# Kernel optimization log

Hardware: AMD Instinct MI355X
Metric: run time of the kernel (lower is better)

Reference implementation:

```python
import jax, jax.numpy as jnp
import numpy as np

B, C, T, H, W = 1, 512, 8, 48, 48
GROUPS = 32
EPS = 1e-6


def setup_inputs() -> dict:
    key = jax.random.key(0)
    ks = jax.random.split(key, 6)
    s = 0.02  # init scale for projection weights
    return {
        "x": jax.random.normal(ks[0], (B, C, T, H, W), dtype=jnp.float32),
        "gamma": jnp.ones((C,), dtype=jnp.float32),
        "beta": jnp.zeros((C,), dtype=jnp.float32),
        "wq": jax.random.normal(ks[1], (C, C), dtype=jnp.float32) * s,
        "bq": jnp.zeros((C,), dtype=jnp.float32),
        "wk": jax.random.normal(ks[2], (C, C), dtype=jnp.float32) * s,
        "bk": jnp.zeros((C,), dtype=jnp.float32),
        "wv": jax.random.normal(ks[3], (C, C), dtype=jnp.float32) * s,
        "bv": jnp.zeros((C,), dtype=jnp.float32),
        "wo": jax.random.normal(ks[4], (C, C), dtype=jnp.float32) * s,
        "bo": jnp.zeros((C,), dtype=jnp.float32),
    }


def _group_norm(x, gamma, beta):
    b, c, t, h, w = x.shape
    xg = x.reshape(b, GROUPS, c // GROUPS, t, h, w)
    mu = xg.mean(axis=(2, 3, 4, 5), keepdims=True)
    var = xg.var(axis=(2, 3, 4, 5), keepdims=True)
    xn = ((xg - mu) * jax.lax.rsqrt(var + EPS)).reshape(b, c, t, h, w)
    return xn * gamma[None, :, None, None, None] + beta[None, :, None, None, None]


def _proj(h, wgt, bias):
    # CausalConv3d with kernel_size=1 == pointwise channel linear
    return jnp.einsum('oc,bcthw->bothw', wgt, h) + bias[None, :, None, None, None]


def reference(x, gamma, beta, wq, bq, wk, bk, wv, bv, wo, bo):
    hn = _group_norm(x, gamma, beta)
    q = _proj(hn, wq, bq)
    k = _proj(hn, wk, bk)
    v = _proj(hn, wv, bv)
    b, c, t, h, w = q.shape
    n = h * w
    # per-frame spatial attention: (b, t, n, c)
    qf = q.transpose(0, 2, 3, 4, 1).reshape(b, t, n, c)
    kf = k.transpose(0, 2, 3, 4, 1).reshape(b, t, n, c)
    vf = v.transpose(0, 2, 3, 4, 1).reshape(b, t, n, c)
    scores = jnp.einsum('btqc,btkc->btqk', qf, kf) * (c ** -0.5)
    attn = jax.nn.softmax(scores, axis=-1)
    of = jnp.einsum('btqk,btkc->btqc', attn, vf)
    o = of.reshape(b, t, h, w, c).transpose(0, 4, 1, 2, 3)
    o = _proj(o, wo, bo)
    return x + o
```

## Files before the change

### kernel.cpp

```cpp
#include <hip/hip_runtime.h>
#include <hip/hip_bf16.h>
#include <cstdint>
#include <type_traits>

typedef __attribute__((ext_vector_type(8))) __bf16 bf16x8;
typedef __attribute__((ext_vector_type(4))) float f32x4;
typedef __attribute__((ext_vector_type(2))) long longx2;

struct bf2frag { bf16x8 k0, k1; };

__device__ __forceinline__ float bf2f(unsigned short u) {
  union { uint32_t i; float f; } v; v.i = (uint32_t)u << 16; return v.f;
}
__device__ __forceinline__ unsigned short f2bf(float f) {
  union { float f; uint32_t i; } v{f};
  uint32_t r = v.i + 0x7fffu + ((v.i >> 16) & 1u);
  return (unsigned short)(r >> 16);
}

__device__ __forceinline__ void gll(const void* g, void* l) {
  __builtin_amdgcn_global_load_lds(
      (const __attribute__((address_space(1))) uint32_t*)(uintptr_t)g,
      (__attribute__((address_space(3))) uint32_t*)(uint32_t)(uintptr_t)l,
      16, 0, 0);
}

__device__ __forceinline__ void bar() {
  asm volatile("" ::: "memory");
  __builtin_amdgcn_s_barrier();
  asm volatile("" ::: "memory");
}

#define VMCNT(n) asm volatile("s_waitcnt vmcnt(" #n ")" ::: "memory")

template <int N>
__device__ __forceinline__ void vmw() {
  if constexpr (N == 0) { VMCNT(0); }
  else if constexpr (N == 1) { VMCNT(1); }
  else if constexpr (N == 2) { VMCNT(2); }
  else if constexpr (N == 3) { VMCNT(3); }
  else if constexpr (N == 4) { VMCNT(4); }
  else if constexpr (N == 5) { VMCNT(5); }
  else if constexpr (N == 6) { VMCNT(6); }
  else if constexpr (N == 7) { VMCNT(7); }
  else if constexpr (N == 8) { VMCNT(8); }
  else if constexpr (N == 9) { VMCNT(9); }
  else if constexpr (N == 10) { VMCNT(10); }
  else { VMCNT(12); }
}

__device__ __forceinline__ f32x4 mma(bf16x8 a, bf16x8 b, f32x4 c) {
  return __builtin_amdgcn_mfma_f32_16x16x32_bf16(a, b, c, 0, 0, 0);
}
__device__ __forceinline__ f32x4 mma(long a, long b, f32x4 c) {
  return __builtin_amdgcn_mfma_f32_16x16x32_fp8_fp8(a, b, c, 0, 0, 0);
}
__device__ __forceinline__ f32x4 mmak(const bf2frag& a, const bf2frag& b, f32x4 c, int k2) {
  return k2 ? mma(a.k1, b.k1, c) : mma(a.k0, b.k0, c);
}
__device__ __forceinline__ f32x4 mmak(longx2 a, longx2 b, f32x4 c, int k2) {
  return mma(a[k2], b[k2], c);
}

__device__ __forceinline__ int perm64(int m) {
  return (m & ~63) | (((m >> 3) & 3) << 4) | (((m >> 5) & 1) << 3) | (m & 7);
}

__global__ __launch_bounds__(256) void stats_partial_k(const float* __restrict__ x,
                                                       float* __restrict__ part) {
  const int g = blockIdx.x >> 3, p = blockIdx.x & 7;
  const float* base = x + (long)g * 16 * 18432 + (long)p * 2304;
  float s = 0.f, ss = 0.f;
  for (int idx = threadIdx.x; idx < 16 * 576; idx += 256) {
    const int c = idx / 576, i4 = idx % 576;
    const float4 v = *(const float4*)(base + (long)c * 18432 + i4 * 4);
    s += v.x + v.y + v.z + v.w;
    ss += v.x * v.x + v.y * v.y + v.z * v.z + v.w * v.w;
  }
  __shared__ float rs[256], rss[256];
  rs[threadIdx.x] = s; rss[threadIdx.x] = ss;
  __syncthreads();
  for (int o = 128; o > 0; o >>= 1) {
    if ((int)threadIdx.x < o) { rs[threadIdx.x] += rs[threadIdx.x + o]; rss[threadIdx.x] += rss[threadIdx.x + o]; }
    __syncthreads();
  }
  if (threadIdx.x == 0) { part[blockIdx.x * 2] = rs[0]; part[blockIdx.x * 2 + 1] = rss[0]; }
}

__global__ __launch_bounds__(256) void gn_transpose_k(const float* __restrict__ x,
                                                      const float* __restrict__ part,
                                                      const float* __restrict__ gamma,
                                                      const float* __restrict__ beta,
                                                      unsigned short* __restrict__ hnT) {
  __shared__ float tile[64][65];
  __shared__ float sm[4], sr[4];
  const int c0 = blockIdx.x * 64, n0 = blockIdx.y * 64;
  const int tn = threadIdx.x & 63, tr = threadIdx.x >> 6;
  if (threadIdx.x < 4) {
    const int g = (c0 >> 4) + threadIdx.x;
    float s = 0.f, ss = 0.f;
    for (int p = 0; p < 8; ++p) { s += part[(g * 8 + p) * 2]; ss += part[(g * 8 + p) * 2 + 1]; }
    const float mean = s / 294912.0f;
    const float var = ss / 294912.0f - mean * mean;
    sm[threadIdx.x] = mean;
    sr[threadIdx.x] = rsqrtf(var + 1e-6f);
  }
  __syncthreads();
  for (int cc = tr; cc < 64; cc += 4) {
    const int c = c0 + cc;
    const float mean = sm[cc >> 4], rstd = sr[cc >> 4];
    const float v = x[(long)c * 18432 + n0 + tn];
    tile[cc][tn] = (v - mean) * rstd * gamma[c] + beta[c];
  }
  __syncthreads();
  for (int nn = tr; nn < 64; nn += 4) {
    hnT[(long)(n0 + nn) * 512 + c0 + tn] = f2bf(tile[tn][nn]);
  }
}

__global__ __launch_bounds__(256) void pack4_bf16_k(const float* __restrict__ w0,
                                                    const float* __restrict__ w1,
                                                    const float* __restrict__ w2,
                                                    const float* __restrict__ w3,
                                                    unsigned short* __restrict__ o0,
                                                    unsigned short* __restrict__ o1,
                                                    unsigned short* __restrict__ o2,
                                                    unsigned short* __restrict__ o3,
                                                    const float* __restrict__ bq,
                                                    const float* __restrict__ bk,
                                                    float* __restrict__ bqk) {
  const int y = blockIdx.y;
  if (y == 4) {
    if (blockIdx.x == 0) {
      const int i = threadIdx.x * 4;
#pragma unroll
      for (int j = 0; j < 4; ++j) {
        const int t = i + j;
        bqk[t] = (t < 512) ? bq[t] : bk[t - 512];
      }
    }
    return;
  }
  const float* w = (y == 0) ? w0 : (y == 1) ? w1 : (y == 2) ? w2 : w3;
  unsigned short* o = (y == 0) ? o0 : (y == 1) ? o1 : (y == 2) ? o2 : o3;
  const int i = (blockIdx.x * 256 + threadIdx.x) * 4;
  const float4 v = *(const float4*)(w + i);
  ushort4 u; u.x = f2bf(v.x); u.y = f2bf(v.y); u.z = f2bf(v.z); u.w = f2bf(v.w);
  *(ushort4*)(o + i) = u;
}

template <int BM, int BIAS_MODE, int OUT_MODE, int STATS, int SCALEN, int MODE, int FP8, int P2,
          int WL = 0, int KU = 1>
__global__ __launch_bounds__((BM == 256 || WL == 2) ? 512 : 256, (WL == 1 && FP8) ? (KU == 2 ? 2 : 4) : 2)
void gemm256(const void* __restrict__ A, long lda, long sAz,
             const void* __restrict__ B, long ldb, long sBz,
             void* __restrict__ Cp, long ldc, long sCz,
             const float* __restrict__ bias,
             const float* __restrict__ resid,
             float* __restrict__ rowsums,
             const float* __restrict__ linv,
             float alpha, int K, int gx, int gy) {
  static_assert(KU == 1 || FP8, "KU=2 only on fp8 path");
  constexpr int EB = FP8 ? 1 : 2;
  constexpr int THREADS = (BM == 256 || WL == 2) ? 512 : 256;
  constexpr int BN = WL ? 128 : 256;
  constexpr int BK = 64 * KU;
  constexpr int HBA = (BM / 2) * BK * EB;
  constexpr int HBB = (BN / 2) * BK * EB;
  constexpr int HBA0 = HBA / KU, HBB0 = HBB / KU;
  constexpr int GA = HBA / (THREADS * 16);
  constexpr int GB = HBB / (THREADS * 16);
  constexpr int GA0 = GA / KU, GB0 = GB / KU;
  constexpr int V0 = GB + 2 * GA, V3 = 2 * GB + GA, VP = GB + GA;
  constexpr int NSLOT = WL ? 8 : ((BM == 256) ? 8 : 4);
  constexpr int NSLOTP = NSLOT + 1;
  constexpr int MR = WL ? 4 : 8;
  constexpr int NR = (WL == 2) ? 2 : 4;
  constexpr int FQ = WL ? 2 : 4;
  constexpr int PRIO = !P2;
  __shared__ alignas(16) unsigned char As[2][2][HBA];
  __shared__ alignas(16) unsigned char Bs[2][2][HBB];
  __shared__ float linvs[SCALEN == 2 ? BN : 1];
  using ABt2 = typename std::conditional<FP8, longx2, bf2frag>::type;

  const int tid = threadIdx.x;
  const int lane = tid & 63, wid = tid >> 6;
  const int wm = (WL == 2) ? (wid >> 2) : (WL ? (wid >> 1) : ((BM == 256) ? (wid & 1) : 0));
  const int wn = (WL == 2) ? (wid & 3) : (WL ? (wid & 1) : ((BM == 256) ? (wid >> 1) : wid));
  int bx, by, bz;
  const void* Asel = A;
  const void* Bsel = B;
  void* Csel = Cp;
  const float* biasSel = bias;
  long ldcSel = ldc;
  bool bias_m = (BIAS_MODE == 1);
  {
    const int g8 = blockIdx.x & 7, n = blockIdx.x >> 3;
    if (MODE == 0) { bz = g8; bx = n % gx; by = n / gx; }
    else if (MODE == 1) { bz = 0; bx = n % gx; by = g8 * gy + n / gx; }
    else if (MODE == 2) { bz = 0; by = n % gy; bx = g8 * gx + n / gy; }
    else {
      bz = 0;
      if ((int)blockIdx.x < gx) {
        bx = n % 8; by = g8 * 18 + n / 8;
      } else {
        const int b2 = (int)blockIdx.x - gx;
        const int g82 = b2 & 7, n2 = b2 >> 3;
        by = n2 % 4; bx = g82 * 18 + n2 / 4;
        Asel = B;
        Bsel = (const void*)resid;
        Csel = (void*)rowsums;
        biasSel = linv;
        ldcSel = 18432;
        bias_m = false;
      }
    }
  }
  const unsigned char* Ab = (const unsigned char*)Asel + ((long)bz * sAz + (long)bx * BM * lda) * EB;
  const unsigned char* Bb = (const unsigned char*)Bsel + ((long)bz * sBz + (long)by * BN * ldb) * EB;

  if constexpr (SCALEN == 2) {
    if (tid < BN) {
      const int ntile = K / BN;
      float L = 0.f;
      for (int xx = 0; xx < ntile; ++xx)
        L += rowsums[((long)(bz * ntile + xx)) * K + by * BN + tid];
      linvs[tid] = 1.0f / L;
    }
  }

  auto stageA = [&](int slot, int h, int k0) {
    if constexpr (!FP8) {
      const int ksw = ((tid & 7) << 3) ^ (((tid >> 3) & 7) << 3);
#pragma unroll
      for (int call = 0; call < GA; ++call) {
        const int r = call * (THREADS / 8) + (tid >> 3);
        const int grow = WL ? (((r >> 5) << 6) + h * 32 + (r & 31))
                            : (((r >> 6) << 7) + h * 64 + (r & 63));
        gll(Ab + ((long)grow * lda + k0) * 2 + ksw * 2, &As[slot][h][call * THREADS * 16 + tid * 16]);
      }
    } else {
#pragma unroll
      for (int call = 0; call < GA; ++call) {
        const int sub = call / GA0, c0 = call % GA0;
        const int l = c0 * (THREADS / 4) + (tid >> 2);
        const int grow = WL ? (((l >> 5) << 6) + h * 32 + (l & 31))
                            : (((l >> 6) << 7) + h * 64 + (l & 63));
        const int x = (((l & 3) ^ ((l >> 2) & 3)) << 4);
        gll(Ab + (long)grow * lda + k0 + sub * 64 + (((tid & 3) << 4) ^ x),
            &As[slot][h][call * THREADS * 16 + tid * 16]);
      }
    }
  };
  auto stageB = [&](int slot, int h, int k0) {
    if constexpr (!FP8) {
      const int ksw = ((tid & 7) << 3) ^ (((tid >> 3) & 7) << 3);
#pragma unroll
      for (int call = 0; call < GB; ++call) {
        const int r = call * (THREADS / 8) + (tid >> 3);
        const int grow = ((r >> 5) << 6) + h * 32 + (r & 31);
        gll(Bb + ((long)grow * ldb + k0) * 2 + ksw * 2, &Bs[slot][h][call * THREADS * 16 + tid * 16]);
      }
    } else {
#pragma unroll
      for (int call = 0; call < GB; ++call) {
        const int sub = call / GB0, c0 = call % GB0;
        const int l = c0 * (THREADS / 4) + (tid >> 2);
        const int grow = ((l >> 5) << 6) + h * 32 + (l & 31);
        const int x = (((l & 3) ^ ((l >> 2) & 3)) << 4);
        gll(Bb + (long)grow * ldb + k0 + sub * 64 + (((tid & 3) << 4) ^ x),
            &Bs[slot][h][call * THREADS * 16 + tid * 16]);
      }
    }
  };
  auto ldA = [&](int slot, int mh, int fq, int sub) -> ABt2 {
    const int r = (WL ? wm * 32 : wm * 64) + fq * 16 + (lane & 15);
    if constexpr (!FP8) {
      bf2frag f;
      const int kk0 = (((lane >> 4) << 3)) ^ ((r & 7) << 3);
      const int kk1 = (32 + ((lane >> 4) << 3)) ^ ((r & 7) << 3);
      f.k0 = *reinterpret_cast<const bf16x8*>(&As[slot][mh][r * 128 + kk0 * 2]);
      f.k1 = *reinterpret_cast<const bf16x8*>(&As[slot][mh][r * 128 + kk1 * 2]);
      return f;
    } else {
      const int x = (((r & 3) ^ ((r >> 2) & 3)) << 4);
      const int kk = ((lane >> 4) << 4) ^ x;
      return *reinterpret_cast<const longx2*>(&As[slot][mh][sub * HBA0 + r * 64 + kk]);
    }
  };
  auto ldB = [&](int slot, int nh, int g, int sub) -> ABt2 {
    const int half = (WL == 2) ? (wn & 1) : nh;
    const int r = ((WL == 2) ? (wn >> 1) : wn) * 32 + g * 16 + (lane & 15);
    if constexpr (!FP8) {
      bf2frag f;
      const int kk0 = (((lane >> 4) << 3)) ^ ((r & 7) << 3);
      const int kk1 = (32 + ((lane >> 4) << 3)) ^ ((r & 7) << 3);
      f.k0 = *reinterpret_cast<const bf16x8*>(&Bs[slot][half][r * 128 + kk0 * 2]);
      f.k1 = *reinterpret_cast<const bf16x8*>(&Bs[slot][half][r * 128 + kk1 * 2]);
      return f;
    } else {
      const int x = (((r & 3) ^ ((r >> 2) & 3)) << 4);
      const int kk = ((lane >> 4) << 4) ^ x;
      return *reinterpret_cast<const longx2*>(&Bs[slot][half][sub * HBB0 + r * 64 + kk]);
    }
  };

  f32x4 acc[MR][NR] = {};
  ABt2 a[FQ * KU], b0[2 * KU], b1[2 * KU];

#define READ_A(SLOT, MH)                                                       \
  _Pragma("unroll") for (int fq = 0; fq < FQ; ++fq)                            \
    _Pragma("unroll") for (int sub = 0; sub < KU; ++sub)                       \
      a[fq * KU + sub] = ldA(SLOT, MH, fq, sub);
#define READ_B(SLOT, NH, DST)                                                  \
  _Pragma("unroll") for (int g = 0; g < 2; ++g)                                \
    _Pragma("unroll") for (int sub = 0; sub < KU; ++sub)                       \
      DST[g * KU + sub] = ldB(SLOT, NH, g, sub);
#define MFMA_QUAD(MH, NH, BARR)                                                \
  if constexpr (PRIO) __builtin_amdgcn_s_setprio(1);                           \
  _Pragma("unroll") for (int fq = 0; fq < FQ; ++fq)                            \
    _Pragma("unroll") for (int g = 0; g < 2; ++g)                              \
      _Pragma("unroll") for (int sub = 0; sub < KU; ++sub)                     \
        _Pragma("unroll") for (int k2 = 0; k2 < 2; ++k2)                       \
          acc[(MH) * FQ + fq][(NH) * 2 + g] =                                  \
              mmak(a[fq * KU + sub], BARR[g * KU + sub],                       \
                   acc[(MH) * FQ + fq][(NH) * 2 + g], k2);                     \
  if constexpr (PRIO) __builtin_amdgcn_s_setprio(0);

  const int KT = K / BK;
  stageB(0, 0, 0);
  stageA(0, 0, 0);
  stageB(0, 1, 0);
  stageA(0, 1, 0);
  stageB(1, 0, BK);
  if constexpr (!P2) stageA(1, 1, BK);
  vmw<VP>();
  bar();

  if constexpr (!P2) {
    for (int W = 0; W < KT; ++W) {
      const int s = W & 1;
      const int kn1 = (W + 1) * BK, kn2 = (W + 2) * BK;
      const bool st1 = (W + 1 < KT), st2 = (W + 2 < KT);
      READ_A(s, 0)
      READ_B(s, 0, b0)
      if (st1) stageA(s ^ 1, 0, kn1);
      bar();
      MFMA_QUAD(0, 0, b0)
      if (st1) { vmw<V0>(); }
      bar();
      READ_B(s, 1, b1)
      if (st1) stageB(s ^ 1, 1, kn1);
      bar();
      MFMA_QUAD(0, 1, b1)
      bar();
      READ_A(s, 1)
      if (st2) stageB(s, 0, kn2);
      bar();
      MFMA_QUAD(1, 1, b1)
      bar();
      if (st2) stageA(s, 1, kn2);
      bar();
      MFMA_QUAD(1, 0, b0)
      if (st2) { vmw<V3>(); } else { vmw<0>(); }
      bar();
    }
  } else {
    for (int W = 0; W < KT; ++W) {
      const int s = W & 1;
      const int kn1 = (W + 1) * BK, kn2 = (W + 2) * BK;
      const bool st1 = (W + 1 < KT), st2 = (W + 2 < KT);
      READ_A(s, 0)
      READ_B(s, 0, b0)
      if constexpr (WL != 2) { READ_B(s, 1, b1) }
      if (st1) { stageA(s ^ 1, 0, kn1); stageB(s ^ 1, 1, kn1); stageA(s ^ 1, 1, kn1); }
      bar();
      MFMA_QUAD(0, 0, b0)
      if constexpr (WL != 2) { MFMA_QUAD(0, 1, b1) }
      if (st1) { vmw<2 * (GA + GB)>(); } else { vmw<0>(); }
      bar();
      READ_A(s, 1)
      if (st2) stageB(s, 0, kn2);
      bar();
      if constexpr (WL != 2) { MFMA_QUAD(1, 1, b1) }
      MFMA_QUAD(1, 0, b0)
      if (st2) { vmw<GA + GB>(); } else if (st1) { vmw<GA>(); } else { vmw<0>(); }
      bar();
    }
  }

  const int mg0 = bx * BM + (WL ? wm * 64 : wm * 128) + ((lane >> 4) << 2);
  const int ng0 = by * BN + ((WL == 2) ? wn * 32 : wn * 64) + (lane & 15);
  float* red = (float*)&As[0][0][0];
#pragma unroll
  for (int N = 0; N < NR; ++N) {
    const int n = ng0 + ((WL == 2) ? N * 16 : ((N >> 1) * 32 + (N & 1) * 16));
    float bn;
    if constexpr (MODE == 3) bn = bias_m ? 0.f : biasSel[n];
    else bn = (BIAS_MODE == 2) ? bias[n] : 0.f;
    const float sc = (SCALEN == 1) ? linv[(long)bz * 2304 + n]
                   : (SCALEN == 2) ? linvs[n - by * BN] : 1.0f;
    float eN = 0.f;
#pragma unroll
    for (int M = 0; M < MR; ++M) {
      const int m = mg0 + (WL ? ((M >> 1) * 32 + (M & 1) * 16) : ((M >> 2) * 64 + (M & 3) * 16));
      const f32x4 av = acc[M][N];
      float vals[4];
#pragma unroll
      for (int j = 0; j < 4; ++j) {
        float addv;
        if constexpr (MODE == 3) addv = bias_m ? biasSel[m + j] : bn;
        else if constexpr (BIAS_MODE == 1) addv = bias[m + j];
        else addv = bn;
        vals[j] = av[j] * alpha + addv;
        if (SCALEN) vals[j] *= sc;
        if (STATS) { vals[j] = __expf(vals[j]); eN += vals[j]; }
      }
      if (OUT_MODE == 0) {
        ushort4 o; o.x = f2bf(vals[0]); o.y = f2bf(vals[1]); o.z = f2bf(vals[2]); o.w = f2bf(vals[3]);
        *(ushort4*)((unsigned short*)Csel + (long)bz * sCz + (long)n * ldcSel + m) = o;
      } else if (OUT_MODE == 2) {
        int pk = __builtin_amdgcn_cvt_pk_fp8_f32(vals[0], vals[1], 0, false);
        pk = __builtin_amdgcn_cvt_pk_fp8_f32(vals[2], vals[3], pk, true);
        *(int*)((unsigned char*)Csel + (long)bz * sCz + (long)n * ldcSel + perm64(m)) = pk;
      } else {
        const float* rp = resid + (long)n * ldcSel + m;
        float4 o; o.x = vals[0] + rp[0]; o.y = vals[1] + rp[1]; o.z = vals[2] + rp[2]; o.w = vals[3] + rp[3];
        *(float4*)((float*)Csel + (long)bz * sCz + (long)n * ldcSel + m) = o;
      }
    }
    if (STATS) {
      const int nloc = n - by * BN;
      const int slot = wm * 4 + (lane >> 4);
      red[nloc * NSLOTP + slot] = eN;
    }
  }
  if (STATS) {
    bar();
    if (tid < BN) {
      float L = 0.f;
#pragma unroll
      for (int s2 = 0; s2 < NSLOT; ++s2) L += red[tid * NSLOTP + s2];
      rowsums[((long)(bz * gx + bx)) * 2304 + by * BN + tid] = L;
    }
  }
#undef READ_A
#undef READ_B
#undef MFMA_QUAD
}

extern "C" void kernel_launch(void* const* d_in, const int* in_sizes, int n_in,
                              void* d_out, int out_size, void* d_ws, size_t ws_size,
                              hipStream_t stream) {
  const float* x = (const float*)d_in[0];
  const float* gamma = (const float*)d_in[1];
  const float* beta = (const float*)d_in[2];
  const float* wq = (const float*)d_in[3];
  const float* bq = (const float*)d_in[4];
  const float* wk = (const float*)d_in[5];
  const float* bk = (const float*)d_in[6];
  const float* wv = (const float*)d_in[7];
  const float* bv = (const float*)d_in[8];
  const float* wo = (const float*)d_in[9];
  const float* bo = (const float*)d_in[10];
  float* out = (float*)d_out;

  char* ws = (char*)d_ws;
  size_t off = 0;
  auto alloc = [&](size_t bytes) {
    char* p = ws + off;
    off = (off + bytes + 255) & ~(size_t)255;
    return p;
  };
  float* part = (float*)alloc(256 * 2 * sizeof(float));
  unsigned short* wqkb = (unsigned short*)alloc((size_t)2 * 262144 * 2);
  unsigned short* wvb = (unsigned short*)alloc((size_t)262144 * 2);
  unsigned short* wob = (unsigned short*)alloc((size_t)262144 * 2);
  float* bqk = (float*)alloc(1024 * sizeof(float));
  float* rowsums = (float*)alloc((size_t)8 * 18 * 2304 * sizeof(float));
  unsigned short* hnT = (unsigned short*)alloc((size_t)18432 * 512 * 2);
  unsigned char* qkA = (unsigned char*)alloc((size_t)18432 * 1024);
  unsigned char* vT = (unsigned char*)alloc((size_t)512 * 18432);
  unsigned char* Sm = (unsigned char*)alloc((size_t)8 * 2304 * 2304);
  unsigned short* Ob = hnT;
  (void)ws_size; (void)in_sizes; (void)n_in; (void)out_size;

  stats_partial_k<<<dim3(256), dim3(256), 0, stream>>>(x, part);
  gn_transpose_k<<<dim3(8, 288), dim3(256), 0, stream>>>(x, part, gamma, beta, hnT);
  pack4_bf16_k<<<dim3(256, 5), dim3(256), 0, stream>>>(wq, wk, wv, wo,
                                                       wqkb, wqkb + 262144, wvb, wob,
                                                       bq, bk, bqk);

  gemm256<128, 1, 2, 0, 0, 3, 0, 1, 2><<<dim3(1728), dim3(512), 0, stream>>>(
      wqkb, 512, 0, hnT, 512, 0, (void*)qkA, 1024, 0, bqk,
      (const float*)wvb, (float*)vT, bv, 1.0f, 512, 1152, 0);
  gemm256<128, 0, 2, 1, 0, 0, 1, 1, 1><<<dim3(2592), dim3(256), 0, stream>>>(
      qkA + 512, 1024, (long)2304 * 1024, qkA, 1024, (long)2304 * 1024, (void*)Sm, 2304,
      (long)2304 * 2304, nullptr, nullptr, rowsums, nullptr,
      0.044194173824159216f, 512, 18, 18);
  gemm256<128, 0, 0, 0, 2, 0, 1, 1, 1><<<dim3(576), dim3(256), 0, stream>>>(
      vT, 18432, 2304, Sm, 2304, (long)2304 * 2304, (void*)Ob, 512, (long)2304 * 512,
      nullptr, nullptr, rowsums, nullptr, 1.0f, 2304, 4, 18);
  gemm256<128, 2, 1, 0, 0, 2, 0, 1, 1><<<dim3(576), dim3(256), 0, stream>>>(
      Ob, 512, 0, wob, 512, 0, (void*)out, 18432, 0, bo, x, nullptr, nullptr,
      1.0f, 512, 18, 4);
}
```

Measured before the change: 210.6 us.

## Run score and output-projection GEMMs with 512-thread WL=2 tiles and lean fp8 staging

Switches the QK^T score GEMM and the output-projection GEMM to the WL=2 variant, which uses 512 threads and smaller per-wave tiles. The fp8 score path gets its own single-load-per-thread staging and a simplified two-half pipeline, plus a higher occupancy hint in its launch bounds. The aim is more waves per CU to hide memory latency. The cost is fewer registers per thread and a different synchronisation pattern that could spill or stall.

Result: no change. 209.9 us (-0.3%).

```diff
diff --git a/kernel.cpp b/kernel.cpp
--- a/kernel.cpp
+++ b/kernel.cpp
@@ -151,7 +151,8 @@
 
 template <int BM, int BIAS_MODE, int OUT_MODE, int STATS, int SCALEN, int MODE, int FP8, int P2,
           int WL = 0, int KU = 1>
-__global__ __launch_bounds__((BM == 256 || WL == 2) ? 512 : 256, (WL == 1 && FP8) ? (KU == 2 ? 2 : 4) : 2)
+__global__ __launch_bounds__((BM == 256 || WL == 2) ? 512 : 256,
+                             (WL == 1 && FP8) ? (KU == 2 ? 2 : 4) : ((WL == 2 && FP8) ? 8 : 2))
 void gemm256(const void* __restrict__ A, long lda, long sAz,
              const void* __restrict__ B, long ldb, long sBz,
              void* __restrict__ Cp, long ldc, long sCz,
@@ -168,9 +169,10 @@
   constexpr int HBA = (BM / 2) * BK * EB;
   constexpr int HBB = (BN / 2) * BK * EB;
   constexpr int HBA0 = HBA / KU, HBB0 = HBB / KU;
-  constexpr int GA = HBA / (THREADS * 16);
-  constexpr int GB = HBB / (THREADS * 16);
-  constexpr int GA0 = GA / KU, GB0 = GB / KU;
+  constexpr bool FT = (WL == 2 && FP8);
+  constexpr int GA = FT ? 1 : HBA / (THREADS * 16);
+  constexpr int GB = FT ? 1 : HBB / (THREADS * 16);
+  constexpr int GA0 = FT ? 1 : GA / KU, GB0 = FT ? 1 : GB / KU;
   constexpr int V0 = GB + 2 * GA, V3 = 2 * GB + GA, VP = GB + GA;
   constexpr int NSLOT = WL ? 8 : ((BM == 256) ? 8 : 4);
   constexpr int NSLOTP = NSLOT + 1;
@@ -273,6 +275,22 @@
       }
     }
   };
+  auto stageAF = [&](int slot, int k0) {
+    const int hh = tid >> 8, tl = tid & 255;
+    const int l = tl >> 2;
+    const int grow = ((l >> 5) << 6) + hh * 32 + (l & 31);
+    const int x = (((l & 3) ^ ((l >> 2) & 3)) << 4);
+    gll(Ab + (long)grow * lda + k0 + (((tid & 3) << 4) ^ x),
+        &As[slot][0][0] + tid * 16);
+  };
+  auto stageBF = [&](int slot, int k0) {
+    const int hh = tid >> 8, tl = tid & 255;
+    const int l = tl >> 2;
+    const int grow = ((l >> 5) << 6) + hh * 32 + (l & 31);
+    const int x = (((l & 3) ^ ((l >> 2) & 3)) << 4);
+    gll(Bb + (long)grow * ldb + k0 + (((tid & 3) << 4) ^ x),
+        &Bs[slot][0][0] + tid * 16);
+  };
   auto ldA = [&](int slot, int mh, int fq, int sub) -> ABt2 {
     const int r = (WL ? wm * 32 : wm * 64) + fq * 16 + (lane & 15);
     if constexpr (!FP8) {
@@ -328,64 +346,89 @@
   if constexpr (PRIO) __builtin_amdgcn_s_setprio(0);
 
   const int KT = K / BK;
-  stageB(0, 0, 0);
-  stageA(0, 0, 0);
-  stageB(0, 1, 0);
-  stageA(0, 1, 0);
-  stageB(1, 0, BK);
-  if constexpr (!P2) stageA(1, 1, BK);
-  vmw<VP>();
-  bar();
-
-  if constexpr (!P2) {
+  if constexpr (FT) {
+    stageAF(0, 0);
+    stageBF(0, 0);
+    stageBF(1, BK);
+    vmw<1>();
+    bar();
     for (int W = 0; W < KT; ++W) {
       const int s = W & 1;
       const int kn1 = (W + 1) * BK, kn2 = (W + 2) * BK;
       const bool st1 = (W + 1 < KT), st2 = (W + 2 < KT);
       READ_A(s, 0)
       READ_B(s, 0, b0)
-      if (st1) stageA(s ^ 1, 0, kn1);
+      if (st1) stageAF(s ^ 1, kn1);
       bar();
       MFMA_QUAD(0, 0, b0)
-      if (st1) { vmw<V0>(); }
-      bar();
-      READ_B(s, 1, b1)
-      if (st1) stageB(s ^ 1, 1, kn1);
-      bar();
-      MFMA_QUAD(0, 1, b1)
       bar();
       READ_A(s, 1)
-      if (st2) stageB(s, 0, kn2);
-      bar();
-      MFMA_QUAD(1, 1, b1)
-      bar();
-      if (st2) stageA(s, 1, kn2);
+      if (st2) stageBF(s, kn2);
       bar();
       MFMA_QUAD(1, 0, b0)
-      if (st2) { vmw<V3>(); } else { vmw<0>(); }
+      if (st2) { vmw<1>(); } else { vmw<0>(); }
       bar();
     }
   } else {
-    for (int W = 0; W < KT; ++W) {
-      const int s = W & 1;
-      const int kn1 = (W + 1) * BK, kn2 = (W + 2) * BK;
-      const bool st1 = (W + 1 < KT), st2 = (W + 2 < KT);
-      READ_A(s, 0)
-      READ_B(s, 0, b0)
-      if constexpr (WL != 2) { READ_B(s, 1, b1) }
-      if (st1) { stageA(s ^ 1, 0, kn1); stageB(s ^ 1, 1, kn1); stageA(s ^ 1, 1, kn1); }
-      bar();
-      MFMA_QUAD(0, 0, b0)
-      if constexpr (WL != 2) { MFMA_QUAD(0, 1, b1) }
-      if (st1) { vmw<2 * (GA + GB)>(); } else { vmw<0>(); }
-      bar();
-      READ_A(s, 1)
-      if (st2) stageB(s, 0, kn2);
-      bar();
-      if constexpr (WL != 2) { MFMA_QUAD(1, 1, b1) }
-      MFMA_QUAD(1, 0, b0)
-      if (st2) { vmw<GA + GB>(); } else if (st1) { vmw<GA>(); } else { vmw<0>(); }
-      bar();
+    stageB(0, 0, 0);
+    stageA(0, 0, 0);
+    stageB(0, 1, 0);
+    stageA(0, 1, 0);
+    stageB(1, 0, BK);
+    if constexpr (!P2) stageA(1, 1, BK);
+    vmw<VP>();
+    bar();
+
+    if constexpr (!P2) {
+      for (int W = 0; W < KT; ++W) {
+        const int s = W & 1;
+        const int kn1 = (W + 1) * BK, kn2 = (W + 2) * BK;
+        const bool st1 = (W + 1 < KT), st2 = (W + 2 < KT);
+        READ_A(s, 0)
+        READ_B(s, 0, b0)
+        if (st1) stageA(s ^ 1, 0, kn1);
+        bar();
+        MFMA_QUAD(0, 0, b0)
+        if (st1) { vmw<V0>(); }
+        bar();
+        READ_B(s, 1, b1)
+        if (st1) stageB(s ^ 1, 1, kn1);
+        bar();
+        MFMA_QUAD(0, 1, b1)
+        bar();
+        READ_A(s, 1)
+        if (st2) stageB(s, 0, kn2);
+        bar();
+        MFMA_QUAD(1, 1, b1)
+        bar();
+        if (st2) stageA(s, 1, kn2);
+        bar();
+        MFMA_QUAD(1, 0, b0)
+        if (st2) { vmw<V3>(); } else { vmw<0>(); }
+        bar();
+      }
+    } else {
+      for (int W = 0; W < KT; ++W) {
+        const int s = W & 1;
+        const int kn1 = (W + 1) * BK, kn2 = (W + 2) * BK;
+        const bool st1 = (W + 1 < KT), st2 = (W + 2 < KT);
+        READ_A(s, 0)
+        READ_B(s, 0, b0)
+        if constexpr (WL != 2) { READ_B(s, 1, b1) }
+        if (st1) { stageA(s ^ 1, 0, kn1); stageB(s ^ 1, 1, kn1); stageA(s ^ 1, 1, kn1); }
+        bar();
+        MFMA_QUAD(0, 0, b0)
+        if constexpr (WL != 2) { MFMA_QUAD(0, 1, b1) }
+        if (st1) { vmw<2 * (GA + GB)>(); } else { vmw<0>(); }
+        bar();
+        READ_A(s, 1)
+        if (st2) stageB(s, 0, kn2);
+        bar();
+        if constexpr (WL != 2) { MFMA_QUAD(1, 1, b1) }
+        MFMA_QUAD(1, 0, b0)
+        if (st2) { vmw<GA + GB>(); } else if (st1) { vmw<GA>(); } else { vmw<0>(); }
+        bar();
+      }
     }
   }
 
@@ -494,14 +537,14 @@
   gemm256<128, 1, 2, 0, 0, 3, 0, 1, 2><<<dim3(1728), dim3(512), 0, stream>>>(
       wqkb, 512, 0, hnT, 512, 0, (void*)qkA, 1024, 0, bqk,
       (const float*)wvb, (float*)vT, bv, 1.0f, 512, 1152, 0);
-  gemm256<128, 0, 2, 1, 0, 0, 1, 1, 1><<<dim3(2592), dim3(256), 0, stream>>>(
+  gemm256<128, 0, 2, 1, 0, 0, 1, 1, 2><<<dim3(2592), dim3(512), 0, stream>>>(
       qkA + 512, 1024, (long)2304 * 1024, qkA, 1024, (long)2304 * 1024, (void*)Sm, 2304,
       (long)2304 * 2304, nullptr, nullptr, rowsums, nullptr,
       0.044194173824159216f, 512, 18, 18);
   gemm256<128, 0, 0, 0, 2, 0, 1, 1, 1><<<dim3(576), dim3(256), 0, stream>>>(
       vT, 18432, 2304, Sm, 2304, (long)2304 * 2304, (void*)Ob, 512, (long)2304 * 512,
       nullptr, nullptr, rowsums, nullptr, 1.0f, 2304, 4, 18);
-  gemm256<128, 2, 1, 0, 0, 2, 0, 1, 1><<<dim3(576), dim3(256), 0, stream>>>(
+  gemm256<128, 2, 1, 0, 0, 2, 0, 1, 2><<<dim3(576), dim3(512), 0, stream>>>(
       Ob, 512, 0, wob, 512, 0, (void*)out, 18432, 0, bo, x, nullptr, nullptr,
       1.0f, 512, 18, 4);
 }
```
